# Kernel optimization log

Measured on AMD Instinct MI355X. Metric: run time of the kernel, lower is better.

## Reference

```python
import jax, jax.numpy as jnp
import numpy as np

N_USERS = 50000
N_ENT = 100000
N_INT = 5
EMB = 128
N_REL = 20
N_EDGES = 1000000
NNZ = 1000000
N_HOPS = 2
C_IDX = jnp.array([0, 1, 2, 3])
V_IDX = jnp.array([4, 5, 6, 7])
K_IDX = jnp.array([8, 9, 10, 11])
O_IDX = jnp.array([12, 13, 14, 15, 16, 17, 18, 19])


def setup_inputs() -> dict:
    key = jax.random.key(0)
    ks = jax.random.split(key, 9)
    return {
        "user_emb": jax.random.normal(ks[0], (N_USERS, EMB), jnp.float32) * 0.1,
        "entity_emb": jax.random.normal(ks[1], (N_ENT, EMB), jnp.float32) * 0.1,
        "intent_emb": jax.random.normal(ks[2], (N_INT, EMB), jnp.float32) * 0.1,
        "edge_index": jax.random.randint(ks[3], (2, N_EDGES), 0, N_ENT),
        "edge_type": jax.random.randint(ks[4], (N_EDGES,), 1, N_REL + 1),
        "interact_rows": jax.random.randint(ks[5], (NNZ,), 0, N_USERS),
        "interact_cols": jax.random.randint(ks[6], (NNZ,), 0, N_ENT),
        "interact_vals": jax.random.uniform(ks[7], (NNZ,), jnp.float32),
        "r_emb": jax.random.normal(ks[8], (N_REL, EMB), jnp.float32) * 0.1,
    }


def _scatter_mean(src, idx, n):
    s = jax.ops.segment_sum(src, idx, num_segments=n)
    c = jax.ops.segment_sum(jnp.ones((src.shape[0],), src.dtype), idx, num_segments=n)
    return jnp.where(c[:, None] > 0, s / jnp.maximum(c, 1.0)[:, None], 0.0)


def _intent_agg(vec, emb):
    # softmax over rows of (vec * emb).sum(-1), then attention-weighted mean
    att = jax.nn.softmax(jnp.sum(vec * emb, axis=1))
    return jnp.mean(att[:, None] * emb, axis=0)


def _l2norm(x):
    n = jnp.linalg.norm(x, axis=1, keepdims=True)
    return x / jnp.maximum(n, 1e-12)


def _dist_cor(t1, t2):
    d = t1.shape[0]
    t1 = t1[:, None]
    t2 = t2[:, None]
    a_ = 2.0 * (t1 @ t1.T)
    b_ = 2.0 * (t2 @ t2.T)
    t1s = t1 ** 2
    t2s = t2 ** 2
    a = jnp.sqrt(jnp.maximum(t1s - a_ + t1s.T, 0.0) + 1e-8)
    b = jnp.sqrt(jnp.maximum(t2s - b_ + t2s.T, 0.0) + 1e-8)
    A = a - a.mean(axis=0, keepdims=True) - a.mean(axis=1, keepdims=True) + a.mean()
    B = b - b.mean(axis=0, keepdims=True) - b.mean(axis=1, keepdims=True) + b.mean()
    d2 = float(d * d)
    dcov_AB = jnp.sqrt(jnp.maximum((A * B).sum() / d2, 0.0) + 1e-8)
    dcov_AA = jnp.sqrt(jnp.maximum((A * A).sum() / d2, 0.0) + 1e-8)
    dcov_BB = jnp.sqrt(jnp.maximum((B * B).sum() / d2, 0.0) + 1e-8)
    return dcov_AB / jnp.sqrt(dcov_AA * dcov_BB + 1e-8)


def _cul_cor(intent_emb):
    cor = 0.0
    for i in range(N_INT):
        for j in range(i + 1, N_INT):
            cor = cor + _dist_cor(intent_emb[i], intent_emb[j])
    return cor


def _forward(user_emb, entity_emb, intent_emb, edge_index, edge_type,
             interact_rows, interact_cols, interact_vals, r_emb):
    head, tail = edge_index[0], edge_index[1]
    cor = _cul_cor(intent_emb)
    res_e, res_u = entity_emb, user_emb
    e, u = entity_emb, user_emb
    for _ in range(N_HOPS):
        # edge gather-multiply-scatter_mean: [E,D]
        msg = e[tail] * r_emb[edge_type - 1]
        e_agg = _scatter_mean(msg, head, N_ENT)
        # intent attention over relation subsets
        all_intent = jnp.stack([
            _intent_agg(intent_emb[0], r_emb),
            _intent_agg(intent_emb[1], r_emb[C_IDX]),
            _intent_agg(intent_emb[2], r_emb[V_IDX]),
            _intent_agg(intent_emb[3], r_emb[K_IDX]),
            _intent_agg(intent_emb[4], r_emb[O_IDX]),
        ], axis=0)
        intent2 = (all_intent + intent_emb) / 2.0  # [5,D]
        # user-intent attention
        score = jax.nn.softmax(u @ intent2.T, axis=1)  # [U,5]
        # sparse.mm(interact_mat, entity_emb)
        u_agg = jax.ops.segment_sum(interact_vals[:, None] * e[interact_cols],
                                    interact_rows, num_segments=N_USERS)
        u_agg = u_agg * (score @ intent2) + u_agg
        e = _l2norm(e_agg)
        u = _l2norm(u_agg)
        res_e = res_e + e
        res_u = res_u + u
    return res_e, res_u, cor


def reference(user_emb, entity_emb, intent_emb, edge_index, edge_type,
              interact_rows, interact_cols, interact_vals, r_emb):
    return _forward(user_emb, entity_emb, intent_emb, edge_index, edge_type,
                    interact_rows, interact_cols, interact_vals, r_emb)
```

## Files before the change

kernel.cpp:

```cpp
#include <hip/hip_runtime.h>
#include <hip/hip_fp16.h>
#include <math.h>

#define N_USERS 50000
#define N_ENT   100000
#define N_INT   5
#define EMB     128
#define N_REL   20
#define N_EDGES 1000000
#define NNZ     1000000
#define SLOT    64
#define NPART   8
#define STAGE_CAP 131072
#define CSTRIDE 32
#define SITEMS  4
#define NCHUNK_S 256
#define EBLOCKS (N_ENT/8)
#define UBLOCKS (N_USERS/8)

union F4H8 { float4 f4; __half2 h2[4]; };

__global__ __launch_bounds__(256) void cor_pair_kernel(const float* __restrict__ intent,
                                                       float* __restrict__ partial) {
    __shared__ float t1[EMB], t2[EMB], rma[EMB], rmb[EMB];
    __shared__ float red[256];
    __shared__ float sh_mean_a, sh_mean_b;
    const int tid = threadIdx.x;
    const int p = blockIdx.x;
    const int pi[10] = {0,0,0,0,1,1,1,2,2,3};
    const int pj[10] = {1,2,3,4,2,3,4,3,4,4};

    if (tid < EMB) {
        t1[tid] = intent[pi[p]*EMB + tid];
        t2[tid] = intent[pj[p]*EMB + tid];
    }
    __syncthreads();
    if (tid < EMB) {
        float x1 = t1[tid], x2 = t2[tid];
        float sa = 0.f, sb = 0.f;
        for (int k = 0; k < EMB; ++k) {
            float da = x1 - t1[k];
            float db = x2 - t2[k];
            sa += sqrtf(da*da + 1e-8f);
            sb += sqrtf(db*db + 1e-8f);
        }
        rma[tid] = sa / (float)EMB;
        rmb[tid] = sb / (float)EMB;
    }
    __syncthreads();
    red[tid] = (tid < EMB) ? rma[tid] : 0.f;
    __syncthreads();
    for (int s = 128; s > 0; s >>= 1) { if (tid < s) red[tid] += red[tid+s]; __syncthreads(); }
    if (tid == 0) sh_mean_a = red[0] / (float)EMB;
    __syncthreads();
    red[tid] = (tid < EMB) ? rmb[tid] : 0.f;
    __syncthreads();
    for (int s = 128; s > 0; s >>= 1) { if (tid < s) red[tid] += red[tid+s]; __syncthreads(); }
    if (tid == 0) sh_mean_b = red[0] / (float)EMB;
    __syncthreads();
    const float mean_a = sh_mean_a, mean_b = sh_mean_b;

    float lab = 0.f, laa = 0.f, lbb = 0.f;
    for (int idx = tid; idx < EMB*EMB; idx += 256) {
        int r = idx >> 7, c = idx & (EMB-1);
        float da = t1[r] - t1[c];
        float db = t2[r] - t2[c];
        float av = sqrtf(da*da + 1e-8f);
        float bv = sqrtf(db*db + 1e-8f);
        float A = av - rma[r] - rma[c] + mean_a;
        float B = bv - rmb[r] - rmb[c] + mean_b;
        lab += A*B; laa += A*A; lbb += B*B;
    }
    red[tid] = lab; __syncthreads();
    for (int s = 128; s > 0; s >>= 1) { if (tid < s) red[tid] += red[tid+s]; __syncthreads(); }
    float sab = red[0]; __syncthreads();
    red[tid] = laa; __syncthreads();
    for (int s = 128; s > 0; s >>= 1) { if (tid < s) red[tid] += red[tid+s]; __syncthreads(); }
    float saa = red[0]; __syncthreads();
    red[tid] = lbb; __syncthreads();
    for (int s = 128; s > 0; s >>= 1) { if (tid < s) red[tid] += red[tid+s]; __syncthreads(); }
    float sbb = red[0]; __syncthreads();

    if (tid == 0) {
        const float d2 = (float)(EMB*EMB);
        float dab = sqrtf(fmaxf(sab/d2, 0.f) + 1e-8f);
        float daa = sqrtf(fmaxf(saa/d2, 0.f) + 1e-8f);
        float dbb = sqrtf(fmaxf(sbb/d2, 0.f) + 1e-8f);
        partial[p] = dab / sqrtf(daa*dbb + 1e-8f);
    }
}

__global__ void cor_sum_kernel(const float* __restrict__ partial, float* __restrict__ out_cor) {
    if (threadIdx.x == 0) {
        float s = 0.f;
        for (int i = 0; i < 10; ++i) s += partial[i];
        out_cor[0] = s;
    }
}

__global__ __launch_bounds__(128) void intent2_kernel(const float* __restrict__ intent,
                                                      const float* __restrict__ r_emb,
                                                      float* __restrict__ intent2) {
    const int i = blockIdx.x;
    const int d = threadIdx.x;
    __shared__ float red[EMB];
    __shared__ float dot[N_REL];
    int start, n;
    if      (i == 0) { start = 0;  n = 20; }
    else if (i == 1) { start = 0;  n = 4;  }
    else if (i == 2) { start = 4;  n = 4;  }
    else if (i == 3) { start = 8;  n = 4;  }
    else             { start = 12; n = 8;  }

    const float v = intent[i*EMB + d];
    for (int j = 0; j < n; ++j) {
        red[d] = v * r_emb[(start+j)*EMB + d];
        __syncthreads();
        for (int s = 64; s > 0; s >>= 1) { if (d < s) red[d] += red[d+s]; __syncthreads(); }
        if (d == 0) dot[j] = red[0];
        __syncthreads();
    }
    float m = -1e30f;
    for (int j = 0; j < n; ++j) m = fmaxf(m, dot[j]);
    float s = 0.f;
    float att[N_REL];
    for (int j = 0; j < n; ++j) { att[j] = expf(dot[j] - m); s += att[j]; }
    float out = 0.f;
    for (int j = 0; j < n; ++j) out += (att[j]/s) * r_emb[(start+j)*EMB + d];
    out /= (float)n;
    intent2[i*EMB + d] = 0.5f * (out + v);
}

__global__ __launch_bounds__(256) void conv_kernel(const float2* __restrict__ in,
                                                   __half2* __restrict__ out, int n) {
    int i = blockIdx.x*256 + threadIdx.x;
    if (i < n) { float2 v = in[i]; out[i] = __floats2half2_rn(v.x, v.y); }
}

__global__ __launch_bounds__(256) void stage_kernel(const int* __restrict__ head,
                                                    const int* __restrict__ tail,
                                                    const int* __restrict__ etype,
                                                    const int* __restrict__ irows,
                                                    const int* __restrict__ icols,
                                                    const float* __restrict__ ivals,
                                                    int* __restrict__ cursor,
                                                    uint2* __restrict__ stage_e,
                                                    uint2* __restrict__ stage_u) {
    __shared__ int l_cnt[2*NPART];
    __shared__ int l_base[2*NPART];
    const int TOTAL = N_EDGES + NNZ;
    const int tid = threadIdx.x;
    const int base = blockIdx.x * (256*SITEMS);

    if (tid < 2*NPART) l_cnt[tid] = 0;
    __syncthreads();

    int part[SITEMS], loc[SITEMS];
    unsigned w0[SITEMS], w1[SITEMS];
    bool act[SITEMS];
    #pragma unroll
    for (int t = 0; t < SITEMS; ++t) {
        const int i = base + t*256 + tid;
        act[t] = i < TOTAL;
        if (act[t]) {
            if (i < N_EDGES) {
                int h = head[i];
                part[t] = h / (N_ENT/NPART);
                w0[t] = (unsigned)h;
                w1[t] = (unsigned)(tail[i] | ((etype[i]-1) << 20));
            } else {
                int j = i - N_EDGES;
                int r = irows[j];
                part[t] = NPART + r / (N_USERS/NPART);
                unsigned q = (unsigned)(ivals[j]*32767.0f + 0.5f);
                w0[t] = (unsigned)r;
                w1[t] = (q << 17) | (unsigned)icols[j];
            }
            loc[t] = atomicAdd(&l_cnt[part[t]], 1);
        }
    }
    __syncthreads();
    if (tid < 2*NPART && l_cnt[tid] > 0)
        l_base[tid] = atomicAdd(&cursor[tid*CSTRIDE], l_cnt[tid]);
    __syncthreads();
    #pragma unroll
    for (int t = 0; t < SITEMS; ++t) {
        if (act[t]) {
            int pos = l_base[part[t]] + loc[t];
            if (pos < STAGE_CAP) {
                if (part[t] < NPART)
                    stage_e[(size_t)part[t]*STAGE_CAP + pos] = make_uint2(w0[t], w1[t]);
                else
                    stage_u[(size_t)(part[t]-NPART)*STAGE_CAP + pos] = make_uint2(w0[t], w1[t]);
            }
        }
    }
}

__global__ __launch_bounds__(256) void scatter_e_kernel(const uint2* __restrict__ stage_e,
                                                        const int* __restrict__ cursor,
                                                        int* __restrict__ cnt_e,
                                                        int* __restrict__ sorted_e) {
    const int part  = blockIdx.x & (NPART-1);
    const int chunk = blockIdx.x >> 3;
    const int n_e = min(cursor[part*CSTRIDE], STAGE_CAP);
    const uint2* se = stage_e + (size_t)part*STAGE_CAP;
    const int i0 = (chunk*256 + threadIdx.x) * 2;
    if (i0 >= n_e) return;
    uint4 v = *(const uint4*)(se + i0);
    int pos0 = atomicAdd(&cnt_e[v.x], 1);
    if (i0 + 1 < n_e) {
        int pos1 = atomicAdd(&cnt_e[v.z], 1);
        if (pos1 < SLOT) sorted_e[(size_t)v.z*SLOT + pos1] = (int)v.w;
    }
    if (pos0 < SLOT) sorted_e[(size_t)v.x*SLOT + pos0] = (int)v.y;
}

__global__ __launch_bounds__(256) void scatter_u_kernel(const uint2* __restrict__ stage_u,
                                                        const int* __restrict__ cursor,
                                                        int* __restrict__ cnt_u,
                                                        unsigned* __restrict__ sorted_u) {
    const int part  = blockIdx.x & (NPART-1);
    const int chunk = blockIdx.x >> 3;
    const int n_u = min(cursor[(NPART+part)*CSTRIDE], STAGE_CAP);
    const uint2* su = stage_u + (size_t)part*STAGE_CAP;
    const int i0 = (chunk*256 + threadIdx.x) * 2;
    if (i0 >= n_u) return;
    uint4 v = *(const uint4*)(su + i0);
    int pos0 = atomicAdd(&cnt_u[v.x], 1);
    if (i0 + 1 < n_u) {
        int pos1 = atomicAdd(&cnt_u[v.z], 1);
        if (pos1 < SLOT) sorted_u[(size_t)v.z*SLOT + pos1] = v.w;
    }
    if (pos0 < SLOT) sorted_u[(size_t)v.x*SLOT + pos0] = v.y;
}

__global__ __launch_bounds__(256) void gather_eu_kernel(const __half2* __restrict__ e_tab,
                                                        const int* __restrict__ cnt_e,
                                                        const int* __restrict__ sorted_e,
                                                        const float* __restrict__ r_emb,
                                                        const float2* __restrict__ base_e,
                                                        float2* __restrict__ res_e,
                                                        __half2* __restrict__ e_out,
                                                        const int* __restrict__ cnt_u,
                                                        const unsigned* __restrict__ sorted_u,
                                                        const float2* __restrict__ u_prev,
                                                        const float* __restrict__ i2,
                                                        const float2* __restrict__ base_u,
                                                        float2* __restrict__ res_u,
                                                        float2* __restrict__ u_out,
                                                        int store, int write_res) {
    __shared__ float2 s_i2[N_INT*64];
    __shared__ float  tr[4][2][132];

    const int wv   = threadIdx.x >> 6;
    const int lane = threadIdx.x & 63;
    const int g = lane >> 4, sl = lane & 15;
    const float4* e4 = (const float4*)e_tab;

    if (blockIdx.x < EBLOCKS) {
        const int row0 = blockIdx.x*8 + wv*2;
        const int row1 = row0 + 1;
        const int deg0 = min(cnt_e[row0], SLOT);
        const int deg1 = min(cnt_e[row1], SLOT);
        int p0 = (lane < deg0) ? sorted_e[(size_t)row0*SLOT + lane] : 0;
        int p1 = (lane < deg1) ? sorted_e[(size_t)row1*SLOT + lane] : 0;

        const float4* r4 = (const float4*)r_emb;
        float accA[8] = {0,0,0,0,0,0,0,0};
        float accB[8] = {0,0,0,0,0,0,0,0};

#define EFMA(ACC, RAW, PM) do { \
            F4H8 u_; u_.f4 = (RAW); \
            const __half* h_ = (const __half*)u_.h2; \
            const int rr_ = (PM) >> 20; \
            float4 w0_ = r4[rr_*32 + sl*2]; \
            float4 w1_ = r4[rr_*32 + sl*2 + 1]; \
            ACC[0] += __half2float(h_[0]) * w0_.x; \
            ACC[1] += __half2float(h_[1]) * w0_.y; \
            ACC[2] += __half2float(h_[2]) * w0_.z; \
            ACC[3] += __half2float(h_[3]) * w0_.w; \
            ACC[4] += __half2float(h_[4]) * w1_.x; \
            ACC[5] += __half2float(h_[5]) * w1_.y; \
            ACC[6] += __half2float(h_[6]) * w1_.z; \
            ACC[7] += __half2float(h_[7]) * w1_.w; \
        } while (0)

        const int dm = max(deg0, deg1);
        for (int k = 0; k < dm; k += 8) {
            const int meA = k + g, meB = k + 4 + g;
            const int pm00 = __shfl(p0, meA), pm01 = __shfl(p0, meB);
            const int pm10 = __shfl(p1, meA), pm11 = __shfl(p1, meB);
            const bool a00 = meA < deg0, a01 = meB < deg0;
            const bool a10 = meA < deg1, a11 = meB < deg1;
            float4 r00, r01, r10, r11;
            if (a00) r00 = e4[(size_t)(pm00 & 0xFFFFF)*16 + sl];
            if (a01) r01 = e4[(size_t)(pm01 & 0xFFFFF)*16 + sl];
            if (a10) r10 = e4[(size_t)(pm10 & 0xFFFFF)*16 + sl];
            if (a11) r11 = e4[(size_t)(pm11 & 0xFFFFF)*16 + sl];
            if (a00) EFMA(accA, r00, pm00);
            if (a01) EFMA(accA, r01, pm01);
            if (a10) EFMA(accB, r10, pm10);
            if (a11) EFMA(accB, r11, pm11);
        }
#undef EFMA

        #pragma unroll
        for (int j = 0; j < 8; ++j) {
            accA[j] += __shfl_xor(accA[j], 16);
            accA[j] += __shfl_xor(accA[j], 32);
            accB[j] += __shfl_xor(accB[j], 16);
            accB[j] += __shfl_xor(accB[j], 32);
        }
        const float invA = (deg0 > 0) ? 1.0f/(float)deg0 : 0.0f;
        const float invB = (deg1 > 0) ? 1.0f/(float)deg1 : 0.0f;
        float ssA = 0.f, ssB = 0.f;
        #pragma unroll
        for (int j = 0; j < 8; ++j) {
            accA[j] *= invA; ssA += accA[j]*accA[j];
            accB[j] *= invB; ssB += accB[j]*accB[j];
        }
        #pragma unroll
        for (int o = 8; o > 0; o >>= 1) {
            ssA += __shfl_xor(ssA, o);
            ssB += __shfl_xor(ssB, o);
        }
        const float invnA = 1.0f / fmaxf(sqrtf(ssA), 1e-12f);
        const float invnB = 1.0f / fmaxf(sqrtf(ssB), 1e-12f);
        #pragma unroll
        for (int j = 0; j < 8; ++j) { accA[j] *= invnA; accB[j] *= invnB; }

#define EPI(ROW, ACC) do { \
            size_t r16 = (size_t)(ROW)*16 + sl; \
            if (store) { \
                F4H8 u_; \
                u_.h2[0] = __floats2half2_rn(ACC[0], ACC[1]); \
                u_.h2[1] = __floats2half2_rn(ACC[2], ACC[3]); \
                u_.h2[2] = __floats2half2_rn(ACC[4], ACC[5]); \
                u_.h2[3] = __floats2half2_rn(ACC[6], ACC[7]); \
                ((float4*)e_out)[r16] = u_.f4; \
            } \
            if (write_res) { \
                F4H8 pv; pv.f4 = ((const float4*)e_tab)[r16]; \
                const float4* b4 = (const float4*)base_e; \
                float4 ba = b4[(size_t)(ROW)*32 + sl*2]; \
                float4 bb = b4[(size_t)(ROW)*32 + sl*2 + 1]; \
                float2 q0 = __half22float2(pv.h2[0]); \
                float2 q1 = __half22float2(pv.h2[1]); \
                float2 q2 = __half22float2(pv.h2[2]); \
                float2 q3 = __half22float2(pv.h2[3]); \
                float4 ra = make_float4(ba.x + q0.x + ACC[0], ba.y + q0.y + ACC[1], \
                                        ba.z + q1.x + ACC[2], ba.w + q1.y + ACC[3]); \
                float4 rb = make_float4(bb.x + q2.x + ACC[4], bb.y + q2.y + ACC[5], \
                                        bb.z + q3.x + ACC[6], bb.w + q3.y + ACC[7]); \
                ((float4*)res_e)[(size_t)(ROW)*32 + sl*2]     = ra; \
                ((float4*)res_e)[(size_t)(ROW)*32 + sl*2 + 1] = rb; \
            } \
        } while (0)

        if (g == 0)      EPI(row0, accA);
        else if (g == 1) EPI(row1, accB);
#undef EPI
    } else {
        for (int k = threadIdx.x; k < N_INT*64; k += 256) s_i2[k] = ((const float2*)i2)[k];
        __syncthreads();
        const int ub = blockIdx.x - EBLOCKS;
        const int row0 = ub*8 + wv*2;
        const int row1 = row0 + 1;
        const int deg0 = min(cnt_u[row0], SLOT);
        const int deg1 = min(cnt_u[row1], SLOT);
        unsigned p0 = (lane < deg0) ? sorted_u[(size_t)row0*SLOT + lane] : 0u;
        unsigned p1 = (lane < deg1) ? sorted_u[(size_t)row1*SLOT + lane] : 0u;

        const float qs = 1.0f/32767.0f;
        float accA[8] = {0,0,0,0,0,0,0,0};
        float accB[8] = {0,0,0,0,0,0,0,0};

#define UFMA(ACC, RAW, Q) do { \
            F4H8 u_; u_.f4 = (RAW); \
            const __half* h_ = (const __half*)u_.h2; \
            const float v_ = (float)((Q) >> 17) * qs; \
            ACC[0] += v_ * __half2float(h_[0]); \
            ACC[1] += v_ * __half2float(h_[1]); \
            ACC[2] += v_ * __half2float(h_[2]); \
            ACC[3] += v_ * __half2float(h_[3]); \
            ACC[4] += v_ * __half2float(h_[4]); \
            ACC[5] += v_ * __half2float(h_[5]); \
            ACC[6] += v_ * __half2float(h_[6]); \
            ACC[7] += v_ * __half2float(h_[7]); \
        } while (0)

        const int dm = max(deg0, deg1);
        for (int k = 0; k < dm; k += 8) {
            const int meA = k + g, meB = k + 4 + g;
            const unsigned q00 = __shfl(p0, meA), q01 = __shfl(p0, meB);
            const unsigned q10 = __shfl(p1, meA), q11 = __shfl(p1, meB);
            const bool a00 = meA < deg0, a01 = meB < deg0;
            const bool a10 = meA < deg1, a11 = meB < deg1;
            float4 r00, r01, r10, r11;
            if (a00) r00 = e4[(size_t)(q00 & 0x1FFFFu)*16 + sl];
            if (a01) r01 = e4[(size_t)(q01 & 0x1FFFFu)*16 + sl];
            if (a10) r10 = e4[(size_t)(q10 & 0x1FFFFu)*16 + sl];
            if (a11) r11 = e4[(size_t)(q11 & 0x1FFFFu)*16 + sl];
            if (a00) UFMA(accA, r00, q00);
            if (a01) UFMA(accA, r01, q01);
            if (a10) UFMA(accB, r10, q10);
            if (a11) UFMA(accB, r11, q11);
        }
#undef UFMA

        #pragma unroll
        for (int j = 0; j < 8; ++j) {
            accA[j] += __shfl_xor(accA[j], 16);
            accA[j] += __shfl_xor(accA[j], 32);
            accB[j] += __shfl_xor(accB[j], 16);
            accB[j] += __shfl_xor(accB[j], 32);
        }
        if (g == 0) {
            #pragma unroll
            for (int j = 0; j < 8; ++j) tr[wv][0][sl*8 + j] = accA[j];
        } else if (g == 1) {
            #pragma unroll
            for (int j = 0; j < 8; ++j) tr[wv][1][sl*8 + j] = accB[j];
        }
        __syncthreads();
        const float s00 = tr[wv][0][2*lane], s01 = tr[wv][0][2*lane + 1];
        const float s10 = tr[wv][1][2*lane], s11 = tr[wv][1][2*lane + 1];

        const size_t o0 = (size_t)row0*64 + lane;
        const size_t o1 = (size_t)row1*64 + lane;
        const float2 up0 = u_prev[o0];
        const float2 up1 = u_prev[o1];
        float dot0[N_INT], dot1[N_INT];
        #pragma unroll
        for (int i = 0; i < N_INT; ++i) {
            float2 w = s_i2[i*64 + lane];
            float pr0 = up0.x*w.x + up0.y*w.y;
            float pr1 = up1.x*w.x + up1.y*w.y;
            #pragma unroll
            for (int o = 32; o > 0; o >>= 1) {
                pr0 += __shfl_xor(pr0, o);
                pr1 += __shfl_xor(pr1, o);
            }
            dot0[i] = pr0; dot1[i] = pr1;
        }
        float m0 = dot0[0], m1 = dot1[0];
        #pragma unroll
        for (int i = 1; i < N_INT; ++i) { m0 = fmaxf(m0, dot0[i]); m1 = fmaxf(m1, dot1[i]); }
        float sm0 = 0.f, sm1 = 0.f;
        #pragma unroll
        for (int i = 0; i < N_INT; ++i) {
            dot0[i] = expf(dot0[i] - m0); sm0 += dot0[i];
            dot1[i] = expf(dot1[i] - m1); sm1 += dot1[i];
        }
        float f00 = 0.f, f01 = 0.f, f10 = 0.f, f11 = 0.f;
        #pragma unroll
        for (int i = 0; i < N_INT; ++i) {
            float a0 = dot0[i] / sm0;
            float a1 = dot1[i] / sm1;
            float2 w = s_i2[i*64 + lane];
            f00 += a0*w.x; f01 += a0*w.y;
            f10 += a1*w.x; f11 += a1*w.y;
        }
        float x00 = s00 * (1.0f + f00), x01 = s01 * (1.0f + f01);
        float x10 = s10 * (1.0f + f10), x11 = s11 * (1.0f + f11);
        float ss0 = x00*x00 + x01*x01;
        float ss1 = x10*x10 + x11*x11;
        #pragma unroll
        for (int o = 32; o > 0; o >>= 1) {
            ss0 += __shfl_xor(ss0, o);
            ss1 += __shfl_xor(ss1, o);
        }
        const float invn0 = 1.0f / fmaxf(sqrtf(ss0), 1e-12f);
        const float invn1 = 1.0f / fmaxf(sqrtf(ss1), 1e-12f);
        x00 *= invn0; x01 *= invn0;
        x10 *= invn1; x11 *= invn1;
        if (store) {
            u_out[o0] = make_float2(x00, x01);
            u_out[o1] = make_float2(x10, x11);
        }
        if (write_res) {
            float2 b0 = base_u[o0];
            float2 b1 = base_u[o1];
            res_u[o0] = make_float2(b0.x + up0.x + x00, b0.y + up0.y + x01);
            res_u[o1] = make_float2(b1.x + up1.x + x10, b1.y + up1.y + x11);
        }
    }
}

extern "C" void kernel_launch(void* const* d_in, const int* in_sizes, int n_in,
                              void* d_out, int out_size, void* d_ws, size_t ws_size,
                              hipStream_t stream) {
    const float* user_emb   = (const float*)d_in[0];
    const float* entity_emb = (const float*)d_in[1];
    const float* intent_emb = (const float*)d_in[2];
    const int*   edge_index = (const int*)  d_in[3];
    const int*   edge_type  = (const int*)  d_in[4];
    const int*   irows      = (const int*)  d_in[5];
    const int*   icols      = (const int*)  d_in[6];
    const float* ivals      = (const float*)d_in[7];
    const float* r_emb      = (const float*)d_in[8];

    float* out     = (float*)d_out;
    float* res_e   = out;
    float* res_u   = out + (size_t)N_ENT*EMB;
    float* out_cor = out + (size_t)N_ENT*EMB + (size_t)N_USERS*EMB;

    const int* head = edge_index;
    const int* tail = edge_index + N_EDGES;

    char* ws = (char*)d_ws;
    __half2* entF16 = (__half2*)ws;  ws += (size_t)N_ENT*EMB*2;
    __half2* eA     = (__half2*)ws;  ws += (size_t)N_ENT*EMB*2;
    float2*  uA     = (float2*)ws;   ws += (size_t)N_USERS*EMB*4;
    int*     sorted_e = (int*)ws;    ws += (size_t)N_ENT*SLOT*4;
    unsigned* sorted_u = (unsigned*)ws; ws += (size_t)N_USERS*SLOT*4;
    int* cnt_e = (int*)ws;           ws += (size_t)N_ENT*4;
    int* cnt_u = (int*)ws;           ws += (size_t)N_USERS*4;
    float* i2  = (float*)ws;         ws += N_INT*EMB*4;
    float* ws_cor = (float*)ws;      ws += 16*4;
    int* cursor = (int*)ws;          ws += 2*NPART*CSTRIDE*4;

    uint2* stage_e = (uint2*)eA;
    uint2* stage_u = (uint2*)uA;

    hipMemsetAsync(cnt_e, 0, (size_t)N_ENT*4, stream);
    hipMemsetAsync(cnt_u, 0, (size_t)N_USERS*4, stream);
    hipMemsetAsync(cursor, 0, 2*NPART*CSTRIDE*4, stream);

    cor_pair_kernel<<<10, 256, 0, stream>>>(intent_emb, ws_cor);
    cor_sum_kernel<<<1, 64, 0, stream>>>(ws_cor, out_cor);
    intent2_kernel<<<N_INT, 128, 0, stream>>>(intent_emb, r_emb, i2);
    conv_kernel<<<(N_ENT*64 + 255)/256, 256, 0, stream>>>((const float2*)entity_emb, entF16, N_ENT*64);

    stage_kernel<<<2048, 256, 0, stream>>>(head, tail, edge_type,
                                           irows, icols, ivals,
                                           cursor, stage_e, stage_u);
    scatter_e_kernel<<<NPART*NCHUNK_S, 256, 0, stream>>>(stage_e, cursor, cnt_e, sorted_e);
    scatter_u_kernel<<<NPART*NCHUNK_S, 256, 0, stream>>>(stage_u, cursor, cnt_u, sorted_u);

    const float2* ent2 = (const float2*)entity_emb;
    const float2* usr2 = (const float2*)user_emb;

    gather_eu_kernel<<<EBLOCKS + UBLOCKS, 256, 0, stream>>>(
        entF16, cnt_e, sorted_e, r_emb, ent2, (float2*)res_e, eA,
        cnt_u, sorted_u, usr2, i2, usr2, (float2*)res_u, uA, 1, 0);

    gather_eu_kernel<<<EBLOCKS + UBLOCKS, 256, 0, stream>>>(
        eA, cnt_e, sorted_e, r_emb, ent2, (float2*)res_e, eA,
        cnt_u, sorted_u, (const float2*)uA, i2, usr2, (float2*)res_u, uA, 0, 1);
}
```

Measured before the change: 503.5 us.

## Merge preprocessing kernels into one launch and fuse entity/user scatter

Folds the correlation, intent aggregation, fp16 conversion and edge staging kernels into one block-partitioned misc kernel. The correlation sum now runs in the last finishing block via an atomic counter. The two scatter kernels become one kernel that handles four items per thread, and three memsets become one over a contiguous zeroed region. The aim is to cut launch count and the serialization gaps between small kernels. In exchange the merged kernel carries extra shared memory and register pressure.

```diff
diff --git a/kernel.cpp b/kernel.cpp
--- a/kernel.cpp
+++ b/kernel.cpp
@@ -14,225 +14,238 @@
 #define STAGE_CAP 131072
 #define CSTRIDE 32
 #define SITEMS  4
-#define NCHUNK_S 256
+#define NCH     128
 #define EBLOCKS (N_ENT/8)
 #define UBLOCKS (N_USERS/8)
 
+#define CORB    10
+#define I2END   (CORB + N_INT)
+#define CONVBLK 3125
+#define CONVEND (I2END + CONVBLK)
+#define STAGBLK 2048
+#define MISCGRID (CONVEND + STAGBLK)
+
 union F4H8 { float4 f4; __half2 h2[4]; };
 
-__global__ __launch_bounds__(256) void cor_pair_kernel(const float* __restrict__ intent,
-                                                       float* __restrict__ partial) {
+__global__ __launch_bounds__(256) void misc_kernel(const float* __restrict__ intent,
+                                                   const float* __restrict__ r_emb,
+                                                   float* __restrict__ i2,
+                                                   float* __restrict__ partial,
+                                                   float* __restrict__ out_cor,
+                                                   int* __restrict__ done,
+                                                   const float2* __restrict__ conv_in,
+                                                   __half2* __restrict__ conv_out,
+                                                   const int* __restrict__ head,
+                                                   const int* __restrict__ tail,
+                                                   const int* __restrict__ etype,
+                                                   const int* __restrict__ irows,
+                                                   const int* __restrict__ icols,
+                                                   const float* __restrict__ ivals,
+                                                   int* __restrict__ cursor,
+                                                   uint2* __restrict__ stage_e,
+                                                   uint2* __restrict__ stage_u) {
     __shared__ float t1[EMB], t2[EMB], rma[EMB], rmb[EMB];
     __shared__ float red[256];
     __shared__ float sh_mean_a, sh_mean_b;
+    __shared__ float dotsh[N_REL];
+    __shared__ int l_cnt[2*NPART];
+    __shared__ int l_base[2*NPART];
     const int tid = threadIdx.x;
-    const int p = blockIdx.x;
-    const int pi[10] = {0,0,0,0,1,1,1,2,2,3};
-    const int pj[10] = {1,2,3,4,2,3,4,3,4,4};
-
-    if (tid < EMB) {
-        t1[tid] = intent[pi[p]*EMB + tid];
-        t2[tid] = intent[pj[p]*EMB + tid];
-    }
-    __syncthreads();
-    if (tid < EMB) {
-        float x1 = t1[tid], x2 = t2[tid];
-        float sa = 0.f, sb = 0.f;
-        for (int k = 0; k < EMB; ++k) {
-            float da = x1 - t1[k];
-            float db = x2 - t2[k];
-            sa += sqrtf(da*da + 1e-8f);
-            sb += sqrtf(db*db + 1e-8f);
-        }
-        rma[tid] = sa / (float)EMB;
-        rmb[tid] = sb / (float)EMB;
-    }
-    __syncthreads();
-    red[tid] = (tid < EMB) ? rma[tid] : 0.f;
-    __syncthreads();
-    for (int s = 128; s > 0; s >>= 1) { if (tid < s) red[tid] += red[tid+s]; __syncthreads(); }
-    if (tid == 0) sh_mean_a = red[0] / (float)EMB;
-    __syncthreads();
-    red[tid] = (tid < EMB) ? rmb[tid] : 0.f;
-    __syncthreads();
-    for (int s = 128; s > 0; s >>= 1) { if (tid < s) red[tid] += red[tid+s]; __syncthreads(); }
-    if (tid == 0) sh_mean_b = red[0] / (float)EMB;
-    __syncthreads();
-    const float mean_a = sh_mean_a, mean_b = sh_mean_b;
-
-    float lab = 0.f, laa = 0.f, lbb = 0.f;
-    for (int idx = tid; idx < EMB*EMB; idx += 256) {
-        int r = idx >> 7, c = idx & (EMB-1);
-        float da = t1[r] - t1[c];
-        float db = t2[r] - t2[c];
-        float av = sqrtf(da*da + 1e-8f);
-        float bv = sqrtf(db*db + 1e-8f);
-        float A = av - rma[r] - rma[c] + mean_a;
-        float B = bv - rmb[r] - rmb[c] + mean_b;
-        lab += A*B; laa += A*A; lbb += B*B;
-    }
-    red[tid] = lab; __syncthreads();
-    for (int s = 128; s > 0; s >>= 1) { if (tid < s) red[tid] += red[tid+s]; __syncthreads(); }
-    float sab = red[0]; __syncthreads();
-    red[tid] = laa; __syncthreads();
-    for (int s = 128; s > 0; s >>= 1) { if (tid < s) red[tid] += red[tid+s]; __syncthreads(); }
-    float saa = red[0]; __syncthreads();
-    red[tid] = lbb; __syncthreads();
-    for (int s = 128; s > 0; s >>= 1) { if (tid < s) red[tid] += red[tid+s]; __syncthreads(); }
-    float sbb = red[0]; __syncthreads();
-
-    if (tid == 0) {
-        const float d2 = (float)(EMB*EMB);
-        float dab = sqrtf(fmaxf(sab/d2, 0.f) + 1e-8f);
-        float daa = sqrtf(fmaxf(saa/d2, 0.f) + 1e-8f);
-        float dbb = sqrtf(fmaxf(sbb/d2, 0.f) + 1e-8f);
-        partial[p] = dab / sqrtf(daa*dbb + 1e-8f);
+
+    if (blockIdx.x < CORB) {
+        const int p = blockIdx.x;
+        const int pi[10] = {0,0,0,0,1,1,1,2,2,3};
+        const int pj[10] = {1,2,3,4,2,3,4,3,4,4};
+
+        if (tid < EMB) {
+            t1[tid] = intent[pi[p]*EMB + tid];
+            t2[tid] = intent[pj[p]*EMB + tid];
+        }
+        __syncthreads();
+        if (tid < EMB) {
+            float x1 = t1[tid], x2 = t2[tid];
+            float sa = 0.f, sb = 0.f;
+            for (int k = 0; k < EMB; ++k) {
+                float da = x1 - t1[k];
+                float db = x2 - t2[k];
+                sa += sqrtf(da*da + 1e-8f);
+                sb += sqrtf(db*db + 1e-8f);
+            }
+            rma[tid] = sa / (float)EMB;
+            rmb[tid] = sb / (float)EMB;
+        }
+        __syncthreads();
+        red[tid] = (tid < EMB) ? rma[tid] : 0.f;
+        __syncthreads();
+        for (int s = 128; s > 0; s >>= 1) { if (tid < s) red[tid] += red[tid+s]; __syncthreads(); }
+        if (tid == 0) sh_mean_a = red[0] / (float)EMB;
+        __syncthreads();
+        red[tid] = (tid < EMB) ? rmb[tid] : 0.f;
+        __syncthreads();
+        for (int s = 128; s > 0; s >>= 1) { if (tid < s) red[tid] += red[tid+s]; __syncthreads(); }
+        if (tid == 0) sh_mean_b = red[0] / (float)EMB;
+        __syncthreads();
+        const float mean_a = sh_mean_a, mean_b = sh_mean_b;
+
+        float lab = 0.f, laa = 0.f, lbb = 0.f;
+        for (int idx = tid; idx < EMB*EMB; idx += 256) {
+            int r = idx >> 7, c = idx & (EMB-1);
+            float da = t1[r] - t1[c];
+            float db = t2[r] - t2[c];
+            float av = sqrtf(da*da + 1e-8f);
+            float bv = sqrtf(db*db + 1e-8f);
+            float A = av - rma[r] - rma[c] + mean_a;
+            float B = bv - rmb[r] - rmb[c] + mean_b;
+            lab += A*B; laa += A*A; lbb += B*B;
+        }
+        red[tid] = lab; __syncthreads();
+        for (int s = 128; s > 0; s >>= 1) { if (tid < s) red[tid] += red[tid+s]; __syncthreads(); }
+        float sab = red[0]; __syncthreads();
+        red[tid] = laa; __syncthreads();
+        for (int s = 128; s > 0; s >>= 1) { if (tid < s) red[tid] += red[tid+s]; __syncthreads(); }
+        float saa = red[0]; __syncthreads();
+        red[tid] = lbb; __syncthreads();
+        for (int s = 128; s > 0; s >>= 1) { if (tid < s) red[tid] += red[tid+s]; __syncthreads(); }
+        float sbb = red[0]; __syncthreads();
+
+        if (tid == 0) {
+            const float d2 = (float)(EMB*EMB);
+            float dab = sqrtf(fmaxf(sab/d2, 0.f) + 1e-8f);
+            float daa = sqrtf(fmaxf(saa/d2, 0.f) + 1e-8f);
+            float dbb = sqrtf(fmaxf(sbb/d2, 0.f) + 1e-8f);
+            partial[p] = dab / sqrtf(daa*dbb + 1e-8f);
+            __threadfence();
+            int t = atomicAdd(done, 1);
+            if (t == CORB - 1) {
+                float s = 0.f;
+                volatile float* vp = (volatile float*)partial;
+                for (int i = 0; i < CORB; ++i) s += vp[i];
+                out_cor[0] = s;
+            }
+        }
+    } else if (blockIdx.x < I2END) {
+        const int i = blockIdx.x - CORB;
+        const int d = tid;
+        int start, n;
+        if      (i == 0) { start = 0;  n = 20; }
+        else if (i == 1) { start = 0;  n = 4;  }
+        else if (i == 2) { start = 4;  n = 4;  }
+        else if (i == 3) { start = 8;  n = 4;  }
+        else             { start = 12; n = 8;  }
+
+        const float v = (d < EMB) ? intent[i*EMB + d] : 0.f;
+        for (int j = 0; j < n; ++j) {
+            if (d < EMB) red[d] = v * r_emb[(start+j)*EMB + d];
+            __syncthreads();
+            for (int s = 64; s > 0; s >>= 1) { if (d < s) red[d] += red[d+s]; __syncthreads(); }
+            if (d == 0) dotsh[j] = red[0];
+            __syncthreads();
+        }
+        if (d < EMB) {
+            float m = -1e30f;
+            for (int j = 0; j < n; ++j) m = fmaxf(m, dotsh[j]);
+            float s = 0.f;
+            float att[N_REL];
+            for (int j = 0; j < n; ++j) { att[j] = expf(dotsh[j] - m); s += att[j]; }
+            float out = 0.f;
+            for (int j = 0; j < n; ++j) out += (att[j]/s) * r_emb[(start+j)*EMB + d];
+            out /= (float)n;
+            i2[i*EMB + d] = 0.5f * (out + v);
+        }
+    } else if (blockIdx.x < CONVEND) {
+        const int base = (blockIdx.x - I2END) * 2048;
+        #pragma unroll
+        for (int t = 0; t < 8; ++t) {
+            int idx = base + t*256 + tid;
+            float2 v = conv_in[idx];
+            conv_out[idx] = __floats2half2_rn(v.x, v.y);
+        }
+    } else {
+        const int TOTAL = N_EDGES + NNZ;
+        const int base = (blockIdx.x - CONVEND) * (256*SITEMS);
+
+        if (tid < 2*NPART) l_cnt[tid] = 0;
+        __syncthreads();
+
+        int part[SITEMS], loc[SITEMS];
+        unsigned w0[SITEMS], w1[SITEMS];
+        bool act[SITEMS];
+        #pragma unroll
+        for (int t = 0; t < SITEMS; ++t) {
+            const int i = base + t*256 + tid;
+            act[t] = i < TOTAL;
+            if (act[t]) {
+                if (i < N_EDGES) {
+                    int h = head[i];
+                    part[t] = h / (N_ENT/NPART);
+                    w0[t] = (unsigned)h;
+                    w1[t] = (unsigned)(tail[i] | ((etype[i]-1) << 20));
+                } else {
+                    int j = i - N_EDGES;
+                    int r = irows[j];
+                    part[t] = NPART + r / (N_USERS/NPART);
+                    unsigned q = (unsigned)(ivals[j]*32767.0f + 0.5f);
+                    w0[t] = (unsigned)r;
+                    w1[t] = (q << 17) | (unsigned)icols[j];
+                }
+                loc[t] = atomicAdd(&l_cnt[part[t]], 1);
+            }
+        }
+        __syncthreads();
+        if (tid < 2*NPART && l_cnt[tid] > 0)
+            l_base[tid] = atomicAdd(&cursor[tid*CSTRIDE], l_cnt[tid]);
+        __syncthreads();
+        #pragma unroll
+        for (int t = 0; t < SITEMS; ++t) {
+            if (act[t]) {
+                int pos = l_base[part[t]] + loc[t];
+                if (pos < STAGE_CAP) {
+                    if (part[t] < NPART)
+                        stage_e[(size_t)part[t]*STAGE_CAP + pos] = make_uint2(w0[t], w1[t]);
+                    else
+                        stage_u[(size_t)(part[t]-NPART)*STAGE_CAP + pos] = make_uint2(w0[t], w1[t]);
+                }
+            }
+        }
     }
 }
 
-__global__ void cor_sum_kernel(const float* __restrict__ partial, float* __restrict__ out_cor) {
-    if (threadIdx.x == 0) {
-        float s = 0.f;
-        for (int i = 0; i < 10; ++i) s += partial[i];
-        out_cor[0] = s;
+__global__ __launch_bounds__(256) void scatter_kernel(const uint2* __restrict__ stage_e,
+                                                      const uint2* __restrict__ stage_u,
+                                                      const int* __restrict__ cursor,
+                                                      int* __restrict__ cnt_e,
+                                                      int* __restrict__ cnt_u,
+                                                      int* __restrict__ sorted_e,
+                                                      unsigned* __restrict__ sorted_u) {
+    const int part = blockIdx.x & (NPART-1);
+    const int cid  = blockIdx.x >> 3;
+    const bool isE = cid < NCH;
+    const int chunk = isE ? cid : cid - NCH;
+    const int n = min(cursor[(isE ? part : NPART + part)*CSTRIDE], STAGE_CAP);
+    const uint2* s = (isE ? stage_e : stage_u) + (size_t)part*STAGE_CAP;
+    int* cnt = isE ? cnt_e : cnt_u;
+
+    const int i0 = (chunk*256 + threadIdx.x) * 4;
+    if (i0 >= n) return;
+    const bool h1 = i0 + 1 < n, h2 = i0 + 2 < n, h3 = i0 + 3 < n;
+    uint4 a = *(const uint4*)(s + i0);
+    uint4 b;
+    if (h2) b = *(const uint4*)(s + i0 + 2);
+    int pos0 = atomicAdd(&cnt[a.x], 1);
+    int pos1 = h1 ? atomicAdd(&cnt[a.z], 1) : 0;
+    int pos2 = h2 ? atomicAdd(&cnt[b.x], 1) : 0;
+    int pos3 = h3 ? atomicAdd(&cnt[b.z], 1) : 0;
+    if (isE) {
+        if (pos0 < SLOT)       sorted_e[(size_t)a.x*SLOT + pos0] = (int)a.y;
+        if (h1 && pos1 < SLOT) sorted_e[(size_t)a.z*SLOT + pos1] = (int)a.w;
+        if (h2 && pos2 < SLOT) sorted_e[(size_t)b.x*SLOT + pos2] = (int)b.y;
+        if (h3 && pos3 < SLOT) sorted_e[(size_t)b.z*SLOT + pos3] = (int)b.w;
+    } else {
+        if (pos0 < SLOT)       sorted_u[(size_t)a.x*SLOT + pos0] = a.y;
+        if (h1 && pos1 < SLOT) sorted_u[(size_t)a.z*SLOT + pos1] = a.w;
+        if (h2 && pos2 < SLOT) sorted_u[(size_t)b.x*SLOT + pos2] = b.y;
+        if (h3 && pos3 < SLOT) sorted_u[(size_t)b.z*SLOT + pos3] = b.w;
     }
-}
-
-__global__ __launch_bounds__(128) void intent2_kernel(const float* __restrict__ intent,
-                                                      const float* __restrict__ r_emb,
-                                                      float* __restrict__ intent2) {
-    const int i = blockIdx.x;
-    const int d = threadIdx.x;
-    __shared__ float red[EMB];
-    __shared__ float dot[N_REL];
-    int start, n;
-    if      (i == 0) { start = 0;  n = 20; }
-    else if (i == 1) { start = 0;  n = 4;  }
-    else if (i == 2) { start = 4;  n = 4;  }
-    else if (i == 3) { start = 8;  n = 4;  }
-    else             { start = 12; n = 8;  }
-
-    const float v = intent[i*EMB + d];
-    for (int j = 0; j < n; ++j) {
-        red[d] = v * r_emb[(start+j)*EMB + d];
-        __syncthreads();
-        for (int s = 64; s > 0; s >>= 1) { if (d < s) red[d] += red[d+s]; __syncthreads(); }
-        if (d == 0) dot[j] = red[0];
-        __syncthreads();
-    }
-    float m = -1e30f;
-    for (int j = 0; j < n; ++j) m = fmaxf(m, dot[j]);
-    float s = 0.f;
-    float att[N_REL];
-    for (int j = 0; j < n; ++j) { att[j] = expf(dot[j] - m); s += att[j]; }
-    float out = 0.f;
-    for (int j = 0; j < n; ++j) out += (att[j]/s) * r_emb[(start+j)*EMB + d];
-    out /= (float)n;
-    intent2[i*EMB + d] = 0.5f * (out + v);
-}
-
-__global__ __launch_bounds__(256) void conv_kernel(const float2* __restrict__ in,
-                                                   __half2* __restrict__ out, int n) {
-    int i = blockIdx.x*256 + threadIdx.x;
-    if (i < n) { float2 v = in[i]; out[i] = __floats2half2_rn(v.x, v.y); }
-}
-
-__global__ __launch_bounds__(256) void stage_kernel(const int* __restrict__ head,
-                                                    const int* __restrict__ tail,
-                                                    const int* __restrict__ etype,
-                                                    const int* __restrict__ irows,
-                                                    const int* __restrict__ icols,
-                                                    const float* __restrict__ ivals,
-                                                    int* __restrict__ cursor,
-                                                    uint2* __restrict__ stage_e,
-                                                    uint2* __restrict__ stage_u) {
-    __shared__ int l_cnt[2*NPART];
-    __shared__ int l_base[2*NPART];
-    const int TOTAL = N_EDGES + NNZ;
-    const int tid = threadIdx.x;
-    const int base = blockIdx.x * (256*SITEMS);
-
-    if (tid < 2*NPART) l_cnt[tid] = 0;
-    __syncthreads();
-
-    int part[SITEMS], loc[SITEMS];
-    unsigned w0[SITEMS], w1[SITEMS];
-    bool act[SITEMS];
-    #pragma unroll
-    for (int t = 0; t < SITEMS; ++t) {
-        const int i = base + t*256 + tid;
-        act[t] = i < TOTAL;
-        if (act[t]) {
-            if (i < N_EDGES) {
-                int h = head[i];
-                part[t] = h / (N_ENT/NPART);
-                w0[t] = (unsigned)h;
-                w1[t] = (unsigned)(tail[i] | ((etype[i]-1) << 20));
-            } else {
-                int j = i - N_EDGES;
-                int r = irows[j];
-                part[t] = NPART + r / (N_USERS/NPART);
-                unsigned q = (unsigned)(ivals[j]*32767.0f + 0.5f);
-                w0[t] = (unsigned)r;
-                w1[t] = (q << 17) | (unsigned)icols[j];
-            }
-            loc[t] = atomicAdd(&l_cnt[part[t]], 1);
-        }
-    }
-    __syncthreads();
-    if (tid < 2*NPART && l_cnt[tid] > 0)
-        l_base[tid] = atomicAdd(&cursor[tid*CSTRIDE], l_cnt[tid]);
-    __syncthreads();
-    #pragma unroll
-    for (int t = 0; t < SITEMS; ++t) {
-        if (act[t]) {
-            int pos = l_base[part[t]] + loc[t];
-            if (pos < STAGE_CAP) {
-                if (part[t] < NPART)
-                    stage_e[(size_t)part[t]*STAGE_CAP + pos] = make_uint2(w0[t], w1[t]);
-                else
-                    stage_u[(size_t)(part[t]-NPART)*STAGE_CAP + pos] = make_uint2(w0[t], w1[t]);
-            }
-        }
-    }
-}
-
-__global__ __launch_bounds__(256) void scatter_e_kernel(const uint2* __restrict__ stage_e,
-                                                        const int* __restrict__ cursor,
-                                                        int* __restrict__ cnt_e,
-                                                        int* __restrict__ sorted_e) {
-    const int part  = blockIdx.x & (NPART-1);
-    const int chunk = blockIdx.x >> 3;
-    const int n_e = min(cursor[part*CSTRIDE], STAGE_CAP);
-    const uint2* se = stage_e + (size_t)part*STAGE_CAP;
-    const int i0 = (chunk*256 + threadIdx.x) * 2;
-    if (i0 >= n_e) return;
-    uint4 v = *(const uint4*)(se + i0);
-    int pos0 = atomicAdd(&cnt_e[v.x], 1);
-    if (i0 + 1 < n_e) {
-        int pos1 = atomicAdd(&cnt_e[v.z], 1);
-        if (pos1 < SLOT) sorted_e[(size_t)v.z*SLOT + pos1] = (int)v.w;
-    }
-    if (pos0 < SLOT) sorted_e[(size_t)v.x*SLOT + pos0] = (int)v.y;
-}
-
-__global__ __launch_bounds__(256) void scatter_u_kernel(const uint2* __restrict__ stage_u,
-                                                        const int* __restrict__ cursor,
-                                                        int* __restrict__ cnt_u,
-                                                        unsigned* __restrict__ sorted_u) {
-    const int part  = blockIdx.x & (NPART-1);
-    const int chunk = blockIdx.x >> 3;
-    const int n_u = min(cursor[(NPART+part)*CSTRIDE], STAGE_CAP);
-    const uint2* su = stage_u + (size_t)part*STAGE_CAP;
-    const int i0 = (chunk*256 + threadIdx.x) * 2;
-    if (i0 >= n_u) return;
-    uint4 v = *(const uint4*)(su + i0);
-    int pos0 = atomicAdd(&cnt_u[v.x], 1);
-    if (i0 + 1 < n_u) {
-        int pos1 = atomicAdd(&cnt_u[v.z], 1);
-        if (pos1 < SLOT) sorted_u[(size_t)v.z*SLOT + pos1] = v.w;
-    }
-    if (pos0 < SLOT) sorted_u[(size_t)v.x*SLOT + pos0] = v.y;
 }
 
 __global__ __launch_bounds__(256) void gather_eu_kernel(const __half2* __restrict__ e_tab,
@@ -515,29 +528,29 @@
     float2*  uA     = (float2*)ws;   ws += (size_t)N_USERS*EMB*4;
     int*     sorted_e = (int*)ws;    ws += (size_t)N_ENT*SLOT*4;
     unsigned* sorted_u = (unsigned*)ws; ws += (size_t)N_USERS*SLOT*4;
+    char* zbase = ws;
     int* cnt_e = (int*)ws;           ws += (size_t)N_ENT*4;
     int* cnt_u = (int*)ws;           ws += (size_t)N_USERS*4;
+    int* cursor = (int*)ws;          ws += 2*NPART*CSTRIDE*4;
+    int* done   = (int*)ws;          ws += 128;
+    size_t zbytes = (size_t)(ws - zbase);
     float* i2  = (float*)ws;         ws += N_INT*EMB*4;
     float* ws_cor = (float*)ws;      ws += 16*4;
-    int* cursor = (int*)ws;          ws += 2*NPART*CSTRIDE*4;
 
     uint2* stage_e = (uint2*)eA;
     uint2* stage_u = (uint2*)uA;
 
-    hipMemsetAsync(cnt_e, 0, (size_t)N_ENT*4, stream);
-    hipMemsetAsync(cnt_u, 0, (size_t)N_USERS*4, stream);
-    hipMemsetAsync(cursor, 0, 2*NPART*CSTRIDE*4, stream);
-
-    cor_pair_kernel<<<10, 256, 0, stream>>>(intent_emb, ws_cor);
-    cor_sum_kernel<<<1, 64, 0, stream>>>(ws_cor, out_cor);
-    intent2_kernel<<<N_INT, 128, 0, stream>>>(intent_emb, r_emb, i2);
-    conv_kernel<<<(N_ENT*64 + 255)/256, 256, 0, stream>>>((const float2*)entity_emb, entF16, N_ENT*64);
-
-    stage_kernel<<<2048, 256, 0, stream>>>(head, tail, edge_type,
-                                           irows, icols, ivals,
-                                           cursor, stage_e, stage_u);
-    scatter_e_kernel<<<NPART*NCHUNK_S, 256, 0, stream>>>(stage_e, cursor, cnt_e, sorted_e);
-    scatter_u_kernel<<<NPART*NCHUNK_S, 256, 0, stream>>>(stage_u, cursor, cnt_u, sorted_u);
+    hipMemsetAsync(zbase, 0, zbytes, stream);
+
+    misc_kernel<<<MISCGRID, 256, 0, stream>>>(intent_emb, r_emb, i2,
+                                              ws_cor, out_cor, done,
+                                              (const float2*)entity_emb, entF16,
+                                              head, tail, edge_type,
+                                              irows, icols, ivals,
+                                              cursor, stage_e, stage_u);
+
+    scatter_kernel<<<NPART*2*NCH, 256, 0, stream>>>(stage_e, stage_u, cursor,
+                                                    cnt_e, cnt_u, sorted_e, sorted_u);
 
     const float2* ent2 = (const float2*)entity_emb;
     const float2* usr2 = (const float2*)user_emb;
```

Result: faster. 449.8 us (-10.7%).
